# Kernel tuning notes

Hardware: AMD Instinct MI355X
Metric: run time of the kernel (lower is better)

The kernel has to match this reference:

```python
import jax, jax.numpy as jnp
import numpy as np

COMMITMENT_COST = 0.25
EPS = 1e-10


def setup_inputs() -> dict:
    key = jax.random.key(0)
    k1, k2 = jax.random.split(key)
    inputs = jax.random.normal(k1, (8192, 8, 8, 8, 8), dtype=jnp.float32)
    codebook = jax.random.normal(k2, (512, 4096), dtype=jnp.float32)  # [E, D]
    return {"inputs": inputs, "codebook": codebook}


def reference(inputs, codebook):
    input_shape = inputs.shape
    B = input_shape[0]
    E, D = codebook.shape
    flat = inputs.reshape(B, -1)  # [B, D], D == embedding_dim

    distances = (
        jnp.sum(flat * flat, axis=1, keepdims=True)
        + jnp.sum(codebook * codebook, axis=1)
        - 2.0 * jnp.matmul(flat, codebook.T)
    )  # [B, E]

    encoding_indices = jnp.argmin(distances, axis=1)  # [B]
    encodings = jax.nn.one_hot(encoding_indices, E, dtype=inputs.dtype)  # [B, E]

    # Gather quantize (same math as encodings @ codebook)
    quantized = jnp.take(codebook, encoding_indices, axis=0).reshape(input_shape)

    e_latent_loss = jnp.mean((jax.lax.stop_gradient(quantized) - inputs) ** 2)
    q_latent_loss = jnp.mean((quantized - jax.lax.stop_gradient(inputs)) ** 2)
    loss = q_latent_loss + COMMITMENT_COST * e_latent_loss

    # Straight-through estimator
    quantized_st = inputs + jax.lax.stop_gradient(quantized - inputs)

    avg_probs = jnp.mean(encodings, axis=0)  # [E]
    perplexity = jnp.exp(-jnp.sum(avg_probs * jnp.log(avg_probs + EPS)))

    return (loss, quantized_st, perplexity, encodings)
```

## Files before the change

kernel.cpp:

```cpp
#include <hip/hip_runtime.h>
#include <stdint.h>

#define B_ROWS 8192
#define DIM 4096
#define E_CODES 512
#define MARGIN 16.0f

typedef __attribute__((ext_vector_type(8))) short short8;
typedef __attribute__((ext_vector_type(4))) float floatx4;
typedef __attribute__((ext_vector_type(4), aligned(4))) float f4u;

#define WS_SCORES 0
#define WS_ENORM  4194304
#define WS_COUNTS 4194816
#define WS_LOSS   4195328

#define O_LOSS 0
#define O_Q    1
#define O_PERP 33554433
#define O_ENC  33554434

__global__ __launch_bounds__(64) void k_enorm(const float* __restrict__ cb, float* __restrict__ enorm) {
    const int e = blockIdx.x;
    const int lane = threadIdx.x;
    const float4* c4 = (const float4*)(cb + (size_t)e * DIM);
    float p = 0.f;
#pragma unroll
    for (int j = 0; j < 16; j++) {
        float4 v = c4[j * 64 + lane];
        p = fmaf(v.x, v.x, fmaf(v.y, v.y, fmaf(v.z, v.z, fmaf(v.w, v.w, p))));
    }
    for (int off = 32; off; off >>= 1) p += __shfl_down(p, off);
    if (lane == 0) enorm[e] = p;
}

__device__ inline uint32_t pk2(float hi, float lo) {
    return __builtin_amdgcn_perm(__float_as_uint(hi), __float_as_uint(lo), 0x07060302u);
}

#define LDK 72
__global__ __launch_bounds__(512) void k_gemm(const float* __restrict__ X, const float* __restrict__ CB,
                                              const float* __restrict__ enorm, float* __restrict__ scores) {
    __shared__ __align__(16) unsigned short As[64 * LDK];
    __shared__ __align__(16) unsigned short Bs[128 * LDK];
    const int bm = blockIdx.x >> 2;
    const int bn = blockIdx.x & 3;
    const int tid = threadIdx.x;
    const int lane = tid & 63;
    const int w = tid >> 6, wr = w >> 2, wc = w & 3;
    const int m16 = lane & 15, q4 = lane >> 4;

    const int rA = tid >> 3, cA = (tid & 7) * 8;
    const int rB = tid >> 2, cB = (tid & 3) * 16;
    const float* xg = X + (size_t)(bm * 64 + rA) * DIM + cA;
    const float* cg = CB + (size_t)(bn * 128 + rB) * DIM + cB;

    floatx4 acc[2][2];
#pragma unroll
    for (int i = 0; i < 2; i++)
#pragma unroll
        for (int j = 0; j < 2; j++) acc[i][j] = (floatx4){0.f, 0.f, 0.f, 0.f};

    for (int kt = 0; kt < DIM; kt += 64) {
        const float4* xa = (const float4*)(xg + kt);
        const float4* ca = (const float4*)(cg + kt);
        float4 xv0 = xa[0], xv1 = xa[1];
        float4 cv0 = ca[0], cv1 = ca[1], cv2 = ca[2], cv3 = ca[3];
        __syncthreads();
        *(uint4*)(&As[rA * LDK + cA]) = make_uint4(pk2(xv0.y, xv0.x), pk2(xv0.w, xv0.z), pk2(xv1.y, xv1.x), pk2(xv1.w, xv1.z));
        *(uint4*)(&Bs[rB * LDK + cB])     = make_uint4(pk2(cv0.y, cv0.x), pk2(cv0.w, cv0.z), pk2(cv1.y, cv1.x), pk2(cv1.w, cv1.z));
        *(uint4*)(&Bs[rB * LDK + cB + 8]) = make_uint4(pk2(cv2.y, cv2.x), pk2(cv2.w, cv2.z), pk2(cv3.y, cv3.x), pk2(cv3.w, cv3.z));
        __syncthreads();
        short8 a[2][2], b[2][2];
#pragma unroll
        for (int i = 0; i < 2; i++)
#pragma unroll
            for (int kk = 0; kk < 2; kk++) {
                a[i][kk] = *(const short8*)(&As[(wr * 32 + i * 16 + m16) * LDK + kk * 32 + q4 * 8]);
                b[i][kk] = *(const short8*)(&Bs[(wc * 32 + i * 16 + m16) * LDK + kk * 32 + q4 * 8]);
            }
#pragma unroll
        for (int kk = 0; kk < 2; kk++)
#pragma unroll
            for (int i = 0; i < 2; i++)
#pragma unroll
                for (int j = 0; j < 2; j++)
                    acc[i][j] = __builtin_amdgcn_mfma_f32_16x16x32_bf16(a[i][kk], b[j][kk], acc[i][j], 0, 0, 0);
    }

#pragma unroll
    for (int j = 0; j < 2; j++) {
        const int col = bn * 128 + wc * 32 + j * 16 + m16;
        const float en = enorm[col];
#pragma unroll
        for (int i = 0; i < 2; i++) {
            const int row0 = bm * 64 + wr * 32 + i * 16 + q4 * 4;
#pragma unroll
            for (int rr = 0; rr < 4; rr++)
                scores[(size_t)(row0 + rr) * E_CODES + col] = en - 2.0f * acc[i][j][rr];
        }
    }
}

__global__ __launch_bounds__(256) void k_fused(const float* __restrict__ X, const float* __restrict__ CB,
                                               const float* __restrict__ scores, int* __restrict__ counts,
                                               float* __restrict__ loss_sum, float* __restrict__ out) {
    const int tid = threadIdx.x;
    const int lane = tid & 63, w = tid >> 6;
    const int row = blockIdx.x * 4 + w;

    const float* sr = scores + (size_t)row * E_CODES;
    float s[8];
#pragma unroll
    for (int g = 0; g < 8; g++) s[g] = sr[g * 64 + lane];

    float mv = s[0]; int mi = lane;
#pragma unroll
    for (int g = 1; g < 8; g++) { if (s[g] < mv) { mv = s[g]; mi = g * 64 + lane; } }
    for (int off = 32; off; off >>= 1) {
        float ov = __shfl_xor(mv, off); int oi = __shfl_xor(mi, off);
        if (ov < mv || (ov == mv && oi < mi)) { mv = ov; mi = oi; }
    }
    const float thr = mv + MARGIN;

    const float4* xr4 = (const float4*)(X + (size_t)row * DIM);
    float4 xv[16];
#pragma unroll
    for (int i = 0; i < 16; i++) xv[i] = xr4[i * 64 + lane];

    float bestd = 3.0e38f; int beste = 1 << 30;
#pragma unroll 1
    for (int g = 0; g < 8; g++) {
        unsigned long long mask = __ballot(s[g] <= thr);
        while (mask) {
            const int b = __builtin_ctzll(mask); mask &= mask - 1;
            const int e = g * 64 + b;
            const float4* cr4 = (const float4*)(CB + (size_t)e * DIM);
            float p = 0.f;
#pragma unroll
            for (int i = 0; i < 16; i++) {
                float4 c = cr4[i * 64 + lane];
                float dx = xv[i].x - c.x, dy = xv[i].y - c.y, dz = xv[i].z - c.z, dw = xv[i].w - c.w;
                p = fmaf(dx, dx, fmaf(dy, dy, fmaf(dz, dz, fmaf(dw, dw, p))));
            }
            for (int off = 32; off; off >>= 1) p += __shfl_xor(p, off);
            if (p < bestd || (p == bestd && e < beste)) { bestd = p; beste = e; }
        }
    }

    const float4* cq4 = (const float4*)(CB + (size_t)beste * DIM);
    f4u* oq4 = (f4u*)(out + O_Q + (size_t)row * DIM);
#pragma unroll
    for (int i = 0; i < 16; i++) {
        float4 x = xv[i], q = cq4[i * 64 + lane];
        f4u r;
        r.x = x.x + (q.x - x.x); r.y = x.y + (q.y - x.y);
        r.z = x.z + (q.z - x.z); r.w = x.w + (q.w - x.w);
        oq4[i * 64 + lane] = r;
    }

    float2* oe2 = (float2*)(out + O_ENC + (size_t)row * E_CODES);
#pragma unroll
    for (int k = 0; k < 4; k++) {
        const int e0 = (k * 64 + lane) * 2;
        float2 v; v.x = (e0 == beste) ? 1.0f : 0.0f; v.y = (e0 + 1 == beste) ? 1.0f : 0.0f;
        oe2[k * 64 + lane] = v;
    }

    if (lane == 0) {
        atomicAdd(&counts[beste], 1);
        atomicAdd(loss_sum, bestd);
    }
}

__global__ __launch_bounds__(512) void k_final(const int* __restrict__ counts, const float* __restrict__ loss_sum,
                                               float* __restrict__ out) {
    const int tid = threadIdx.x;
    const int lane = tid & 63, w = tid >> 6;
    __shared__ float r[8];
    const float p = (float)counts[tid] * (1.0f / 8192.0f);
    float h = p * logf(p + 1e-10f);
    for (int off = 32; off; off >>= 1) h += __shfl_down(h, off);
    if (lane == 0) r[w] = h;
    __syncthreads();
    if (tid == 0) {
        float H = 0.f;
        for (int k = 0; k < 8; k++) H += r[k];
        out[O_PERP] = expf(-H);
        out[O_LOSS] = loss_sum[0] * (1.25f / 33554432.0f);
    }
}

extern "C" void kernel_launch(void* const* d_in, const int* in_sizes, int n_in,
                              void* d_out, int out_size, void* d_ws, size_t ws_size,
                              hipStream_t stream) {
    const float* X  = (const float*)d_in[0];
    const float* CB = (const float*)d_in[1];
    float* out = (float*)d_out;
    float* ws  = (float*)d_ws;
    float* scores = ws + WS_SCORES;
    float* enorm  = ws + WS_ENORM;
    int*   counts = (int*)(ws + WS_COUNTS);
    float* loss_s = ws + WS_LOSS;

    hipMemsetAsync(counts, 0, (E_CODES + 1) * sizeof(int), stream);

    k_enorm<<<E_CODES, 64, 0, stream>>>(CB, enorm);
    k_gemm<<<512, 512, 0, stream>>>(X, CB, enorm, scores);
    k_fused<<<B_ROWS / 4, 256, 0, stream>>>(X, CB, scores, counts, loss_s, out);
    k_final<<<1, 512, 0, stream>>>(counts, loss_s, out);
}
```

Measured before the change: 468.1 us.

## Split-K GEMM with atomics, skip refinement for unique candidates, fold x-norm into loss

The GEMM is split into two K halves across 1024 blocks, with a swizzled tile order, and partial products are accumulated into zero-initialised scores with float atomics. The scoring kernel now adds the codebook norms itself. The exact-distance refinement is skipped when only one candidate lies within the margin. The loss is rebuilt from the bf16 scores plus a global x-norm sum computed inside the GEMM, and the quantized output is written as a plain copy of the codebook row. This adds a memset of the 16MB score buffer and atomic traffic, and computing the loss from bf16 dot products may change its precision.

```diff
diff --git a/kernel.cpp b/kernel.cpp
--- a/kernel.cpp
+++ b/kernel.cpp
@@ -8,12 +8,12 @@
 
 typedef __attribute__((ext_vector_type(8))) short short8;
 typedef __attribute__((ext_vector_type(4))) float floatx4;
-typedef __attribute__((ext_vector_type(4), aligned(4))) float f4u;
 
 #define WS_SCORES 0
 #define WS_ENORM  4194304
 #define WS_COUNTS 4194816
 #define WS_LOSS   4195328
+#define WS_XNORM  4195329
 
 #define O_LOSS 0
 #define O_Q    1
@@ -40,11 +40,15 @@
 
 #define LDK 72
 __global__ __launch_bounds__(512) void k_gemm(const float* __restrict__ X, const float* __restrict__ CB,
-                                              const float* __restrict__ enorm, float* __restrict__ scores) {
+                                              float* __restrict__ scores, float* __restrict__ xnorm_sum) {
     __shared__ __align__(16) unsigned short As[64 * LDK];
     __shared__ __align__(16) unsigned short Bs[128 * LDK];
-    const int bm = blockIdx.x >> 2;
-    const int bn = blockIdx.x & 3;
+    __shared__ float xred[8];
+    const int id = blockIdx.x;
+    const int ks = id >> 9;
+    const int h = id & 511;
+    const int bn = (h >> 3) & 3;
+    const int bm = ((h >> 5) << 3) | (h & 7);
     const int tid = threadIdx.x;
     const int lane = tid & 63;
     const int w = tid >> 6, wr = w >> 2, wc = w & 3;
@@ -52,20 +56,23 @@
 
     const int rA = tid >> 3, cA = (tid & 7) * 8;
     const int rB = tid >> 2, cB = (tid & 3) * 16;
-    const float* xg = X + (size_t)(bm * 64 + rA) * DIM + cA;
-    const float* cg = CB + (size_t)(bn * 128 + rB) * DIM + cB;
+    const float* xg = X + (size_t)(bm * 64 + rA) * DIM + cA + (ks << 11);
+    const float* cg = CB + (size_t)(bn * 128 + rB) * DIM + cB + (ks << 11);
 
     floatx4 acc[2][2];
 #pragma unroll
     for (int i = 0; i < 2; i++)
 #pragma unroll
         for (int j = 0; j < 2; j++) acc[i][j] = (floatx4){0.f, 0.f, 0.f, 0.f};
-
-    for (int kt = 0; kt < DIM; kt += 64) {
+    float xn = 0.f;
+
+    for (int kt = 0; kt < 2048; kt += 64) {
         const float4* xa = (const float4*)(xg + kt);
         const float4* ca = (const float4*)(cg + kt);
         float4 xv0 = xa[0], xv1 = xa[1];
         float4 cv0 = ca[0], cv1 = ca[1], cv2 = ca[2], cv3 = ca[3];
+        xn = fmaf(xv0.x, xv0.x, fmaf(xv0.y, xv0.y, fmaf(xv0.z, xv0.z, fmaf(xv0.w, xv0.w, xn))));
+        xn = fmaf(xv1.x, xv1.x, fmaf(xv1.y, xv1.y, fmaf(xv1.z, xv1.z, fmaf(xv1.w, xv1.w, xn))));
         __syncthreads();
         *(uint4*)(&As[rA * LDK + cA]) = make_uint4(pk2(xv0.y, xv0.x), pk2(xv0.w, xv0.z), pk2(xv1.y, xv1.x), pk2(xv1.w, xv1.z));
         *(uint4*)(&Bs[rB * LDK + cB])     = make_uint4(pk2(cv0.y, cv0.x), pk2(cv0.w, cv0.z), pk2(cv1.y, cv1.x), pk2(cv1.w, cv1.z));
@@ -91,20 +98,29 @@
 #pragma unroll
     for (int j = 0; j < 2; j++) {
         const int col = bn * 128 + wc * 32 + j * 16 + m16;
-        const float en = enorm[col];
 #pragma unroll
         for (int i = 0; i < 2; i++) {
             const int row0 = bm * 64 + wr * 32 + i * 16 + q4 * 4;
 #pragma unroll
             for (int rr = 0; rr < 4; rr++)
-                scores[(size_t)(row0 + rr) * E_CODES + col] = en - 2.0f * acc[i][j][rr];
+                atomicAdd(&scores[(size_t)(row0 + rr) * E_CODES + col], acc[i][j][rr]);
         }
     }
+
+    for (int off = 32; off; off >>= 1) xn += __shfl_down(xn, off);
+    if (lane == 0) xred[w] = xn;
+    __syncthreads();
+    if (tid == 0) {
+        float s = 0.f;
+        for (int k = 0; k < 8; k++) s += xred[k];
+        atomicAdd(xnorm_sum, s);
+    }
 }
 
 __global__ __launch_bounds__(256) void k_fused(const float* __restrict__ X, const float* __restrict__ CB,
-                                               const float* __restrict__ scores, int* __restrict__ counts,
-                                               float* __restrict__ loss_sum, float* __restrict__ out) {
+                                               const float* __restrict__ scores, const float* __restrict__ enorm,
+                                               int* __restrict__ counts, float* __restrict__ loss_sum,
+                                               float* __restrict__ out) {
     const int tid = threadIdx.x;
     const int lane = tid & 63, w = tid >> 6;
     const int row = blockIdx.x * 4 + w;
@@ -112,7 +128,7 @@
     const float* sr = scores + (size_t)row * E_CODES;
     float s[8];
 #pragma unroll
-    for (int g = 0; g < 8; g++) s[g] = sr[g * 64 + lane];
+    for (int g = 0; g < 8; g++) s[g] = enorm[g * 64 + lane] - 2.0f * sr[g * 64 + lane];
 
     float mv = s[0]; int mi = lane;
 #pragma unroll
@@ -123,41 +139,39 @@
     }
     const float thr = mv + MARGIN;
 
-    const float4* xr4 = (const float4*)(X + (size_t)row * DIM);
-    float4 xv[16];
-#pragma unroll
-    for (int i = 0; i < 16; i++) xv[i] = xr4[i * 64 + lane];
-
-    float bestd = 3.0e38f; int beste = 1 << 30;
+    unsigned long long bal[8]; int nc = 0;
+#pragma unroll
+    for (int g = 0; g < 8; g++) { bal[g] = __ballot(s[g] <= thr); nc += __popcll(bal[g]); }
+
+    int beste = mi;
+    if (nc > 1) {
+        const float4* xr4 = (const float4*)(X + (size_t)row * DIM);
+        float bestd = 3.0e38f; beste = 1 << 30;
 #pragma unroll 1
-    for (int g = 0; g < 8; g++) {
-        unsigned long long mask = __ballot(s[g] <= thr);
-        while (mask) {
-            const int b = __builtin_ctzll(mask); mask &= mask - 1;
-            const int e = g * 64 + b;
-            const float4* cr4 = (const float4*)(CB + (size_t)e * DIM);
-            float p = 0.f;
-#pragma unroll
-            for (int i = 0; i < 16; i++) {
-                float4 c = cr4[i * 64 + lane];
-                float dx = xv[i].x - c.x, dy = xv[i].y - c.y, dz = xv[i].z - c.z, dw = xv[i].w - c.w;
-                p = fmaf(dx, dx, fmaf(dy, dy, fmaf(dz, dz, fmaf(dw, dw, p))));
+        for (int g = 0; g < 8; g++) {
+            unsigned long long mask = bal[g];
+            while (mask) {
+                const int b = __builtin_ctzll(mask); mask &= mask - 1;
+                const int e = g * 64 + b;
+                const float4* cr4 = (const float4*)(CB + (size_t)e * DIM);
+                float p = 0.f;
+#pragma unroll
+                for (int i = 0; i < 16; i++) {
+                    float4 x = xr4[i * 64 + lane];
+                    float4 c = cr4[i * 64 + lane];
+                    float dx = x.x - c.x, dy = x.y - c.y, dz = x.z - c.z, dw = x.w - c.w;
+                    p = fmaf(dx, dx, fmaf(dy, dy, fmaf(dz, dz, fmaf(dw, dw, p))));
+                }
+                for (int off = 32; off; off >>= 1) p += __shfl_xor(p, off);
+                if (p < bestd || (p == bestd && e < beste)) { bestd = p; beste = e; }
             }
-            for (int off = 32; off; off >>= 1) p += __shfl_xor(p, off);
-            if (p < bestd || (p == bestd && e < beste)) { bestd = p; beste = e; }
         }
     }
 
-    const float4* cq4 = (const float4*)(CB + (size_t)beste * DIM);
-    f4u* oq4 = (f4u*)(out + O_Q + (size_t)row * DIM);
-#pragma unroll
-    for (int i = 0; i < 16; i++) {
-        float4 x = xv[i], q = cq4[i * 64 + lane];
-        f4u r;
-        r.x = x.x + (q.x - x.x); r.y = x.y + (q.y - x.y);
-        r.z = x.z + (q.z - x.z); r.w = x.w + (q.w - x.w);
-        oq4[i * 64 + lane] = r;
-    }
+    const float* cq = CB + (size_t)beste * DIM;
+    float* oq = out + O_Q + (size_t)row * DIM;
+#pragma unroll
+    for (int i = 0; i < 64; i++) oq[i * 64 + lane] = cq[i * 64 + lane];
 
     float2* oe2 = (float2*)(out + O_ENC + (size_t)row * E_CODES);
 #pragma unroll
@@ -169,12 +183,13 @@
 
     if (lane == 0) {
         atomicAdd(&counts[beste], 1);
-        atomicAdd(loss_sum, bestd);
+        const float ssel = enorm[beste] - 2.0f * sr[beste];
+        atomicAdd(loss_sum, ssel);
     }
 }
 
 __global__ __launch_bounds__(512) void k_final(const int* __restrict__ counts, const float* __restrict__ loss_sum,
-                                               float* __restrict__ out) {
+                                               const float* __restrict__ xnorm_sum, float* __restrict__ out) {
     const int tid = threadIdx.x;
     const int lane = tid & 63, w = tid >> 6;
     __shared__ float r[8];
@@ -187,7 +202,8 @@
         float H = 0.f;
         for (int k = 0; k < 8; k++) H += r[k];
         out[O_PERP] = expf(-H);
-        out[O_LOSS] = loss_sum[0] * (1.25f / 33554432.0f);
+        const float dist_total = loss_sum[0] + 0.25f * xnorm_sum[0];
+        out[O_LOSS] = dist_total * (1.25f / 33554432.0f);
     }
 }
 
@@ -202,11 +218,13 @@
     float* enorm  = ws + WS_ENORM;
     int*   counts = (int*)(ws + WS_COUNTS);
     float* loss_s = ws + WS_LOSS;
-
-    hipMemsetAsync(counts, 0, (E_CODES + 1) * sizeof(int), stream);
+    float* xnorm  = ws + WS_XNORM;
+
+    hipMemsetAsync(scores, 0, (size_t)B_ROWS * E_CODES * sizeof(float), stream);
+    hipMemsetAsync(counts, 0, (E_CODES + 2) * sizeof(int), stream);
 
     k_enorm<<<E_CODES, 64, 0, stream>>>(CB, enorm);
-    k_gemm<<<512, 512, 0, stream>>>(X, CB, enorm, scores);
-    k_fused<<<B_ROWS / 4, 256, 0, stream>>>(X, CB, scores, counts, loss_s, out);
-    k_final<<<1, 512, 0, stream>>>(counts, loss_s, out);
-}
+    k_gemm<<<1024, 512, 0, stream>>>(X, CB, scores, xnorm);
+    k_fused<<<B_ROWS / 4, 256, 0, stream>>>(X, CB, scores, enorm, counts, loss_s, out);
+    k_final<<<1, 512, 0, stream>>>(counts, loss_s, xnorm, out);
+}
```

After: 502.5 us. 7.3% more time.
